# Kernel optimization log

Measured on AMD Instinct MI355X. Metric: run time of the kernel, lower is better.

## Reference

```python
import jax, jax.numpy as jnp
import numpy as np

BETA_MIN = 0.01
BETA_MAX = 0.995
EPS = 1e-6


def setup_inputs() -> dict:
    key = jax.random.key(0)
    k1, k2, k3, k4 = jax.random.split(key, 4)
    B, T, D = 16, 4096, 128
    return {
        "q": jax.random.normal(k1, (B, T, D), dtype=jnp.float32),
        "k": jax.random.normal(k2, (B, T, D), dtype=jnp.float32),
        "v": jax.random.normal(k3, (B, T, D), dtype=jnp.float32),
        "beta": jax.random.uniform(k4, (B, T, 1), dtype=jnp.float32),
        "mask": jnp.ones((B, T, 1), dtype=jnp.float32),
        "base_beta_1": jnp.asarray(2.0, dtype=jnp.float32),
        "base_beta_2": jnp.asarray(3.0, dtype=jnp.float32),
    }


def _delta_scan(q, k, v, beta, mask, base_beta_1, base_beta_2):
    B, T, D = q.shape
    phi_q = jax.nn.elu(q) + 1.0  # positive feature map
    phi_k = jax.nn.elu(k) + 1.0
    b1_base = jnp.clip(jax.nn.sigmoid(base_beta_1), BETA_MIN, BETA_MAX)
    b2_base = jnp.clip(jax.nn.sigmoid(base_beta_2), BETA_MIN, BETA_MAX)

    # time-major for scan: [T, B, ...]
    xs = (
        jnp.swapaxes(phi_q, 0, 1),
        jnp.swapaxes(phi_k, 0, 1),
        jnp.swapaxes(v, 0, 1),
        jnp.swapaxes(beta, 0, 1),
        jnp.swapaxes(mask, 0, 1),
    )

    H1 = jnp.zeros((B, D, D), dtype=q.dtype)
    H2 = jnp.zeros((B, D, D), dtype=q.dtype)
    Z1 = jnp.zeros((B, D), dtype=q.dtype)
    Z2 = jnp.zeros((B, D), dtype=q.dtype)

    def step(carry, x):
        H1, H2, Z1, Z2 = carry
        q_t, k_t, v_t, b_in_t, m_t = x  # q_t:[B,D], b_in_t/m_t:[B,1]
        b_in_t = jnp.clip(b_in_t, BETA_MIN, BETA_MAX)
        b1_t = jnp.clip(b1_base * b_in_t, BETA_MIN, BETA_MAX)  # [B,1]
        b2_t = jnp.clip(b2_base * b_in_t, BETA_MIN, BETA_MAX)
        kv = jnp.einsum('bd,be->bde', k_t, v_t) * m_t[:, :, None]  # masked outer product
        H1 = H1 * b1_t[:, :, None] + kv
        H2 = H2 * b2_t[:, :, None] + kv
        Z1 = Z1 * b1_t + k_t * m_t
        Z2 = Z2 * b2_t + k_t * m_t
        num = jnp.einsum('bd,bde->be', q_t, H1 + H2)
        den = jnp.maximum(jnp.sum(q_t * (Z1 + Z2), axis=-1, keepdims=True), EPS)
        o_t = num / den * m_t
        return (H1, H2, Z1, Z2), o_t

    _, outs = jax.lax.scan(step, (H1, H2, Z1, Z2), xs)
    return jnp.swapaxes(outs, 0, 1)  # [B, T, D]


def reference(q, k, v, beta, mask, base_beta_1, base_beta_2):
    return _delta_scan(q, k, v, beta, mask, base_beta_1, base_beta_2)
```

## Files before the change

### kernel.cpp

```cpp
#include <hip/hip_runtime.h>

#define B_ 16
#define T_ 4096
#define D_ 128
#define L_ 128
#define NC_ 32
#define CH_ (B_*NC_)
#define LDK 136
#define LDP 136

typedef __attribute__((ext_vector_type(8))) short bf16x8;
typedef __attribute__((ext_vector_type(4))) float f32x4;

__device__ __forceinline__ float clampf(float x, float lo, float hi) {
    return fminf(fmaxf(x, lo), hi);
}
__device__ __forceinline__ float phi_f(float x) {
    return x > 0.f ? x + 1.f : __expf(x);
}
__device__ __forceinline__ unsigned short bf16r(float f) {
    unsigned u = __builtin_bit_cast(unsigned, f);
    u += 0x7FFFu + ((u >> 16) & 1u);
    return (unsigned short)(u >> 16);
}
__device__ __forceinline__ float fbf(unsigned short h) {
    unsigned u = ((unsigned)h) << 16; return __builtin_bit_cast(float, u);
}
__device__ __forceinline__ unsigned pack2bf(float a, float b) {
    return (unsigned)bf16r(a) | ((unsigned)bf16r(b) << 16);
}
__device__ __forceinline__ uint4 pack8(const float* f) {
    uint4 r;
    r.x = pack2bf(f[0], f[1]); r.y = pack2bf(f[2], f[3]);
    r.z = pack2bf(f[4], f[5]); r.w = pack2bf(f[6], f[7]);
    return r;
}
__device__ __forceinline__ f32x4 zero4() { f32x4 z; z[0]=0.f; z[1]=0.f; z[2]=0.f; z[3]=0.f; return z; }


__global__ __launch_bounds__(256, 2) void kA(
        const float* __restrict__ beta,
        const float* __restrict__ bb1, const float* __restrict__ bb2,
        const float* __restrict__ kk, const float* __restrict__ vv,
        const float* __restrict__ mask,
        float* __restrict__ lg1, float* __restrict__ lg2,
        unsigned short* __restrict__ phiKT, unsigned short* __restrict__ VtT,
        unsigned short* __restrict__ Cws, float* __restrict__ zc) {
    int ch = blockIdx.x;
    int b = ch / NC_, c = ch % NC_;
    int tbase = b * T_ + c * L_;
    int tid = threadIdx.x, lane = tid & 63, w = tid >> 6;
    int l15 = lane & 15, lg4 = lane >> 4;
    size_t cb = (size_t)ch * (D_ * L_);

    __shared__ float s1[L_], s2[L_];
    __shared__ float wL[2][L_];
    __shared__ float sZp[2][256];
    __shared__ unsigned short sKrm[128 * LDK];
    __shared__ unsigned short sVrm[128 * LDK];

    int t = tid & 127;
    if (tid < 128) {
        float b1b = clampf(1.f / (1.f + __expf(-bb1[0])), 0.01f, 0.995f);
        float b2b = clampf(1.f / (1.f + __expf(-bb2[0])), 0.01f, 0.995f);
        float be = clampf(beta[tbase + t], 0.01f, 0.995f);
        s1[t] = __logf(clampf(b1b * be, 0.01f, 0.995f));
        s2[t] = __logf(clampf(b2b * be, 0.01f, 0.995f));
    }
    __syncthreads();
    for (int off = 1; off < L_; off <<= 1) {
        float a1 = 0.f, a2 = 0.f;
        if (tid < 128 && t >= off) { a1 = s1[t - off]; a2 = s2[t - off]; }
        __syncthreads();
        if (tid < 128) { s1[t] += a1; s2[t] += a2; }
        __syncthreads();
    }
    if (tid < 128) {
        lg1[tbase + t] = s1[t]; lg2[tbase + t] = s2[t];
        float tot1 = s1[L_ - 1], tot2 = s2[L_ - 1];
    }
    __syncthreads();
    if (tid < 128) {
        wL[0][t] = __expf(s1[L_ - 1] - s1[t]);
        wL[1][t] = __expf(s2[L_ - 1] - s2[t]);
    }

#pragma unroll
    for (int p = 0; p < 8; ++p) {
        int i = tid + p * 256;
        int s = i >> 4, dg = i & 15, d0 = dg * 8;
        const float* kp = &kk[(size_t)(tbase + s) * D_ + d0];
        float4 x0 = *(const float4*)kp;
        float4 x1 = *(const float4*)(kp + 4);
        float m = mask[tbase + s];
        float pq[8] = {phi_f(x0.x)*m, phi_f(x0.y)*m, phi_f(x0.z)*m, phi_f(x0.w)*m,
                       phi_f(x1.x)*m, phi_f(x1.y)*m, phi_f(x1.z)*m, phi_f(x1.w)*m};
        uint4 pk = pack8(pq);
        *(uint4*)&sKrm[s * LDK + d0] = pk;
        *(uint4*)&phiKT[cb + (size_t)((((s >> 4) * 4 + (d0 >> 5)) * 64 + ((d0 >> 3) & 3) * 16 + (s & 15)) * 8)] = pk;
    }
#pragma unroll
    for (int p = 0; p < 8; ++p) {
        int i = tid + p * 256;
        int s = i >> 4, eg = i & 15, e0 = eg * 8;
        const float* vp = &vv[(size_t)(tbase + s) * D_ + e0];
        float4 x0 = *(const float4*)vp;
        float4 x1 = *(const float4*)(vp + 4);
        float pv8[8] = {x0.x, x0.y, x0.z, x0.w, x1.x, x1.y, x1.z, x1.w};
        *(uint4*)&sVrm[s * LDK + e0] = pack8(pv8);
    }
    __syncthreads();

#pragma unroll
    for (int p = 0; p < 2; ++p) {
        int i = tid + p * 256;
        int mg = i >> 6, ln = i & 63;
        int vg4 = ln >> 4, v15 = ln & 15;
#pragma unroll
        for (int ks = 0; ks < 4; ++ks) {
            unsigned short u[8];
#pragma unroll
            for (int j = 0; j < 8; ++j)
                u[j] = sVrm[(ks * 32 + vg4 * 8 + j) * LDK + mg * 16 + v15];
            uint4 r;
            r.x = (unsigned)u[0] | ((unsigned)u[1] << 16);
            r.y = (unsigned)u[2] | ((unsigned)u[3] << 16);
            r.z = (unsigned)u[4] | ((unsigned)u[5] << 16);
            r.w = (unsigned)u[6] | ((unsigned)u[7] << 16);
            *(uint4*)&VtT[cb + (size_t)(((mg * 4 + ks) * 64 + ln) * 8)] = r;
        }
    }

    {
        int zd = tid & 127, zh = tid >> 7;
        float z0 = 0.f, z1 = 0.f;
#pragma unroll
        for (int ss = 0; ss < 64; ++ss) {
            int s = zh * 64 + ss;
            float kv = fbf(sKrm[s * LDK + zd]);
            z0 += wL[0][s] * kv;
            z1 += wL[1][s] * kv;
        }
        sZp[0][tid] = z0; sZp[1][tid] = z1;
    }

    f32x4 acc[2][2][8];
#pragma unroll
    for (int st = 0; st < 2; ++st)
#pragma unroll
        for (int mm = 0; mm < 2; ++mm)
#pragma unroll
            for (int n = 0; n < 8; ++n) acc[st][mm][n] = zero4();

#pragma unroll
    for (int ks = 0; ks < 4; ++ks) {
        int koff = ks * 32 + lg4 * 8;
        float4 w0a = *(const float4*)&wL[0][koff];
        float4 w0b = *(const float4*)&wL[0][koff + 4];
        float4 w1a = *(const float4*)&wL[1][koff];
        float4 w1b = *(const float4*)&wL[1][koff + 4];
        float wl0[8] = {w0a.x, w0a.y, w0a.z, w0a.w, w0b.x, w0b.y, w0b.z, w0b.w};
        float wl1[8] = {w1a.x, w1a.y, w1a.z, w1a.w, w1b.x, w1b.y, w1b.z, w1b.w};
        bf16x8 as[2][2];
#pragma unroll
        for (int mm = 0; mm < 2; ++mm) {
#pragma unroll
            for (int j = 0; j < 8; ++j) {
                float av = fbf(sVrm[(koff + j) * LDK + (w * 2 + mm) * 16 + l15]);
                as[0][mm][j] = (short)bf16r(av * wl0[j]);
                as[1][mm][j] = (short)bf16r(av * wl1[j]);
            }
        }
#pragma unroll
        for (int n = 0; n < 8; ++n) {
            bf16x8 bb;
#pragma unroll
            for (int j = 0; j < 8; ++j)
                bb[j] = (short)sKrm[(koff + j) * LDK + n * 16 + l15];
#pragma unroll
            for (int st = 0; st < 2; ++st)
#pragma unroll
                for (int mm = 0; mm < 2; ++mm)
                    acc[st][mm][n] = __builtin_amdgcn_mfma_f32_16x16x32_bf16(as[st][mm], bb, acc[st][mm][n], 0, 0, 0);
        }
    }
    __syncthreads();
    if (tid < 128) {
        zc[((size_t)(0 * B_ + b) * NC_ + c) * D_ + tid] = sZp[0][tid] + sZp[0][tid + 128];
        zc[((size_t)(1 * B_ + b) * NC_ + c) * D_ + tid] = sZp[1][tid] + sZp[1][tid + 128];
    }

#pragma unroll
    for (int st = 0; st < 2; ++st) {
        unsigned short* Cp = Cws + ((size_t)(st * B_ + b) * NC_ + c) * (D_ * D_);
#pragma unroll
        for (int mm = 0; mm < 2; ++mm)
#pragma unroll
            for (int n = 0; n < 8; ++n)
#pragma unroll
                for (int r = 0; r < 4; ++r) {
                    int e = (w * 2 + mm) * 16 + lg4 * 4 + r;
                    int d = n * 16 + l15;
                    Cp[(size_t)((((e >> 4) * 4 + (d >> 5)) * 64 + ((d >> 3) & 3) * 16 + (e & 15)) * 8 + (d & 7))] = bf16r(acc[st][mm][n][r]);
                }
    }
}

__global__ void k2f(unsigned short* __restrict__ Cws, float* __restrict__ zc,
                    const float* __restrict__ lg1, const float* __restrict__ lg2) {
    int g = blockIdx.x * blockDim.x + threadIdx.x;
    if (g < 131072) {
        int st = g >> 16;
        int rem = g & 65535;
        int b = rem >> 12;
        int de = (rem & 4095) * 4;
        const float* lg = st ? lg2 : lg1;
        size_t base = ((size_t)(st * B_ + b) * NC_) * (D_ * D_) + de;
        float run0 = 0.f, run1 = 0.f, run2 = 0.f, run3 = 0.f;
        for (int c = 0; c < NC_; c++) {
            float a = __expf(lg[b * T_ + c * L_ + L_ - 1]);
            uint2 val = *(uint2*)&Cws[base + (size_t)c * (D_ * D_)];
            float t0 = fbf((unsigned short)(val.x & 0xffff)), t1 = fbf((unsigned short)(val.x >> 16));
            float t2 = fbf((unsigned short)(val.y & 0xffff)), t3 = fbf((unsigned short)(val.y >> 16));
            uint2 wv; wv.x = pack2bf(run0, run1); wv.y = pack2bf(run2, run3);
            *(uint2*)&Cws[base + (size_t)c * (D_ * D_)] = wv;
            run0 = a * run0 + t0; run1 = a * run1 + t1;
            run2 = a * run2 + t2; run3 = a * run3 + t3;
        }
    } else {
        int gz = g - 131072;
        int st = gz >> 11;
        int rem = gz & 2047;
        int b = rem >> 7;
        int d = rem & 127;
        const float* lg = st ? lg2 : lg1;
        size_t base = ((size_t)(st * B_ + b) * NC_) * D_ + d;
        float run = 0.f;
        for (int c = 0; c < NC_; c++) {
            float a = __expf(lg[b * T_ + c * L_ + L_ - 1]);
            float tmp = zc[base + (size_t)c * D_];
            zc[base + (size_t)c * D_] = run;
            run = a * run + tmp;
        }
    }
}

__global__ __launch_bounds__(256, 2) void k3_v6(
        const float* __restrict__ qq, const float* __restrict__ mask,
        const float* __restrict__ lg1, const float* __restrict__ lg2,
        const unsigned short* __restrict__ phiKT, const unsigned short* __restrict__ VtT,
        const unsigned short* __restrict__ Cws, const float* __restrict__ zc,
        float* __restrict__ out) {
    __shared__ unsigned short bufP[4][32 * LDP];
    int ch = blockIdx.x;
    int b = ch / NC_, c = ch % NC_;
    int tbase = b * T_ + c * L_;
    int tid = threadIdx.x, lane = tid & 63, w = tid >> 6;
    int l15 = lane & 15, lg4 = lane >> 4;
    unsigned short* bufPw = &bufP[w][0];
    size_t cb = (size_t)ch * 16384;

    int trow0 = w * 16 + l15, trow1 = 64 + trow0;
    size_t gt0 = (size_t)(tbase + trow0), gt1 = (size_t)(tbase + trow1);

    float lg1t0 = lg1[gt0], lg2t0 = lg2[gt0], mt0 = mask[gt0];
    float lg1t1 = lg1[gt1], lg2t1 = lg2[gt1], mt1 = mask[gt1];
    float a1t0 = __expf(lg1t0), a2t0 = __expf(lg2t0);
    float a1t1 = __expf(lg1t1), a2t1 = __expf(lg2t1);

    bf16x8 qf0[4], qf1[4];
#pragma unroll
    for (int ks = 0; ks < 4; ++ks) {
        int koff = ks * 32 + lg4 * 8;
        const float* qp0 = &qq[gt0 * D_ + koff];
        const float* qp1 = &qq[gt1 * D_ + koff];
        float4 x0 = *(const float4*)qp0, x1 = *(const float4*)(qp0 + 4);
        float4 y0 = *(const float4*)qp1, y1 = *(const float4*)(qp1 + 4);
        float p0[8] = {phi_f(x0.x), phi_f(x0.y), phi_f(x0.z), phi_f(x0.w),
                       phi_f(x1.x), phi_f(x1.y), phi_f(x1.z), phi_f(x1.w)};
        float p1[8] = {phi_f(y0.x), phi_f(y0.y), phi_f(y0.z), phi_f(y0.w),
                       phi_f(y1.x), phi_f(y1.y), phi_f(y1.z), phi_f(y1.w)};
#pragma unroll
        for (int j = 0; j < 8; ++j) {
            qf0[ks][j] = (short)bf16r(p0[j]);
            qf1[ks][j] = (short)bf16r(p1[j]);
        }
    }

    const float* z1p = &zc[((size_t)(0 * B_ + b) * NC_ + c) * D_];
    const float* z2p = &zc[((size_t)(1 * B_ + b) * NC_ + c) * D_];
    float d1_0 = 0.f, d2_0 = 0.f, d1_1 = 0.f, d2_1 = 0.f;
#pragma unroll
    for (int ks = 0; ks < 4; ++ks) {
        int off = ks * 32 + lg4 * 8;
        float4 za = *(const float4*)(z1p + off), zb = *(const float4*)(z1p + off + 4);
        float4 zca = *(const float4*)(z2p + off), zcb = *(const float4*)(z2p + off + 4);
        float z1a[8] = {za.x, za.y, za.z, za.w, zb.x, zb.y, zb.z, zb.w};
        float z2a[8] = {zca.x, zca.y, zca.z, zca.w, zcb.x, zcb.y, zcb.z, zcb.w};
#pragma unroll
        for (int j = 0; j < 8; ++j) {
            float fq0 = fbf((unsigned short)qf0[ks][j]);
            float fq1 = fbf((unsigned short)qf1[ks][j]);
            d1_0 += fq0 * z1a[j]; d2_0 += fq0 * z2a[j];
            d1_1 += fq1 * z1a[j]; d2_1 += fq1 * z2a[j];
        }
    }
    d1_0 += __shfl_xor(d1_0, 16); d1_0 += __shfl_xor(d1_0, 32);
    d2_0 += __shfl_xor(d2_0, 16); d2_0 += __shfl_xor(d2_0, 32);
    d1_1 += __shfl_xor(d1_1, 16); d1_1 += __shfl_xor(d1_1, 32);
    d2_1 += __shfl_xor(d2_1, 16); d2_1 += __shfl_xor(d2_1, 32);

    float rs0 = 0.f, rs1 = 0.f;
#pragma unroll
    for (int mh = 0; mh < 2; ++mh) {
        bf16x8 kf[16];
#pragma unroll
        for (int mm = 0; mm < 4; ++mm)
#pragma unroll
            for (int ks = 0; ks < 4; ++ks)
                kf[mm * 4 + ks] = *(const bf16x8*)&phiKT[cb + (size_t)(((((mh * 4 + mm) * 4) + ks) * 64 + lane) * 8)];
        f32x4 acc0[4], acc1[4];
#pragma unroll
        for (int mm = 0; mm < 4; ++mm) { acc0[mm] = zero4(); acc1[mm] = zero4(); }
#pragma unroll
        for (int ks = 0; ks < 4; ++ks)
#pragma unroll
            for (int mm = 0; mm < 4; ++mm) {
                if (mh == 0)
                    acc0[mm] = __builtin_amdgcn_mfma_f32_16x16x32_bf16(kf[mm * 4 + ks], qf0[ks], acc0[mm], 0, 0, 0);
                acc1[mm] = __builtin_amdgcn_mfma_f32_16x16x32_bf16(kf[mm * 4 + ks], qf1[ks], acc1[mm], 0, 0, 0);
            }
#pragma unroll
        for (int mm = 0; mm < 4; ++mm) {
            int s0 = (mh * 4 + mm) * 16 + lg4 * 4;
            float4 l1s = *(const float4*)&lg1[tbase + s0];
            float4 l2s = *(const float4*)&lg2[tbase + s0];
            float l1a[4] = {l1s.x, l1s.y, l1s.z, l1s.w};
            float l2a[4] = {l2s.x, l2s.y, l2s.z, l2s.w};
            if (mh == 0) {
                float pv[4];
#pragma unroll
                for (int r = 0; r < 4; ++r) {
                    int s = s0 + r;
                    float p = 0.f;
                    if (s <= trow0)
                        p = acc0[mm][r] * (__expf(lg1t0 - l1a[r]) + __expf(lg2t0 - l2a[r]));
                    pv[r] = p; rs0 += p;
                }
                uint2 dd; dd.x = pack2bf(pv[0], pv[1]); dd.y = pack2bf(pv[2], pv[3]);
                *(uint2*)&bufPw[l15 * LDP + s0] = dd;
            }
            {
                float pv[4];
#pragma unroll
                for (int r = 0; r < 4; ++r) {
                    int s = s0 + r;
                    float p = 0.f;
                    if (s <= trow1)
                        p = acc1[mm][r] * (__expf(lg1t1 - l1a[r]) + __expf(lg2t1 - l2a[r]));
                    pv[r] = p; rs1 += p;
                }
                uint2 dd; dd.x = pack2bf(pv[0], pv[1]); dd.y = pack2bf(pv[2], pv[3]);
                *(uint2*)&bufPw[(16 + l15) * LDP + s0] = dd;
            }
        }
    }
    rs0 += __shfl_xor(rs0, 16); rs0 += __shfl_xor(rs0, 32);
    rs1 += __shfl_xor(rs1, 16); rs1 += __shfl_xor(rs1, 32);
    float osc0 = mt0 / fmaxf(a1t0 * d1_0 + a2t0 * d2_0 + rs0, 1e-6f);
    float osc1 = mt1 / fmaxf(a1t1 * d1_1 + a2t1 * d2_1 + rs1, 1e-6f);

    f32x4 acc_o0[8], acc_o1[8];
#pragma unroll
    for (int m = 0; m < 8; ++m) { acc_o0[m] = zero4(); acc_o1[m] = zero4(); }
#pragma unroll
    for (int st = 0; st < 2; ++st) {
        const unsigned short* Hp = Cws + ((size_t)(st * B_ + b) * NC_ + c) * (D_ * D_);
        float sc0 = st ? a2t0 : a1t0;
        float sc1 = st ? a2t1 : a1t1;
#pragma unroll
        for (int ks2 = 0; ks2 < 2; ++ks2) {
            bf16x8 hf[16];
#pragma unroll
            for (int kq = 0; kq < 2; ++kq)
#pragma unroll
                for (int m = 0; m < 8; ++m)
                    hf[kq * 8 + m] = *(const bf16x8*)&Hp[(size_t)(((m * 4 + ks2 * 2 + kq) * 64 + lane) * 8)];
#pragma unroll
            for (int kq = 0; kq < 2; ++kq) {
                int ks = ks2 * 2 + kq;
                bf16x8 qs0, qs1;
#pragma unroll
                for (int j = 0; j < 8; ++j) {
                    qs0[j] = (short)bf16r(fbf((unsigned short)qf0[ks][j]) * sc0);
                    qs1[j] = (short)bf16r(fbf((unsigned short)qf1[ks][j]) * sc1);
                }
#pragma unroll
                for (int m = 0; m < 8; ++m) {
                    acc_o0[m] = __builtin_amdgcn_mfma_f32_16x16x32_bf16(hf[kq * 8 + m], qs0, acc_o0[m], 0, 0, 0);
                    acc_o1[m] = __builtin_amdgcn_mfma_f32_16x16x32_bf16(hf[kq * 8 + m], qs1, acc_o1[m], 0, 0, 0);
                }
            }
        }
    }

#pragma unroll
    for (int ks = 0; ks < 4; ++ks) {
        bf16x8 vf[8];
#pragma unroll
        for (int m = 0; m < 8; ++m)
            vf[m] = *(const bf16x8*)&VtT[cb + (size_t)(((m * 4 + ks) * 64 + lane) * 8)];
        bf16x8 pf1 = *(const bf16x8*)&bufPw[(16 + l15) * LDP + ks * 32 + lg4 * 8];
        if (ks < 2) {
            bf16x8 pf0 = *(const bf16x8*)&bufPw[l15 * LDP + ks * 32 + lg4 * 8];
#pragma unroll
            for (int m = 0; m < 8; ++m)
                acc_o0[m] = __builtin_amdgcn_mfma_f32_16x16x32_bf16(vf[m], pf0, acc_o0[m], 0, 0, 0);
        }
#pragma unroll
        for (int m = 0; m < 8; ++m)
            acc_o1[m] = __builtin_amdgcn_mfma_f32_16x16x32_bf16(vf[m], pf1, acc_o1[m], 0, 0, 0);
    }

#pragma unroll
    for (int m = 0; m < 8; ++m) {
        float4 o0, o1;
        o0.x = acc_o0[m][0] * osc0; o0.y = acc_o0[m][1] * osc0;
        o0.z = acc_o0[m][2] * osc0; o0.w = acc_o0[m][3] * osc0;
        o1.x = acc_o1[m][0] * osc1; o1.y = acc_o1[m][1] * osc1;
        o1.z = acc_o1[m][2] * osc1; o1.w = acc_o1[m][3] * osc1;
        *(float4*)&out[gt0 * D_ + m * 16 + lg4 * 4] = o0;
        *(float4*)&out[gt1 * D_ + m * 16 + lg4 * 4] = o1;
    }
}

extern "C" void kernel_launch(void* const* d_in, const int* in_sizes, int n_in,
                              void* d_out, int out_size, void* d_ws, size_t ws_size,
                              hipStream_t stream) {
    const float* q    = (const float*)d_in[0];
    const float* k    = (const float*)d_in[1];
    const float* v    = (const float*)d_in[2];
    const float* beta = (const float*)d_in[3];
    const float* mask = (const float*)d_in[4];
    const float* bb1  = (const float*)d_in[5];
    const float* bb2  = (const float*)d_in[6];
    float* out = (float*)d_out;

    size_t n_lg = (size_t)B_ * T_;
    size_t n_z  = (size_t)2 * B_ * NC_ * D_;
    size_t n_C  = (size_t)2 * B_ * NC_ * D_ * D_;
    size_t n_kt = (size_t)B_ * T_ * D_;
    size_t need = (2 * n_lg + n_z) * sizeof(float) + (n_C + 2 * n_kt) * sizeof(unsigned short);
    if (ws_size < need) return;

    float* lg1 = (float*)d_ws;
    float* lg2 = lg1 + n_lg;
    float* zc  = lg2 + n_lg;
    unsigned short* Cws   = (unsigned short*)(zc + n_z);
    unsigned short* phiKT = Cws + n_C;
    unsigned short* VtT   = phiKT + n_kt;

    kA<<<CH_, 256, 0, stream>>>(beta, bb1, bb2, k, v, mask, lg1, lg2, phiKT, VtT, Cws, zc);
    k2f<<<528, 256, 0, stream>>>(Cws, zc, lg1, lg2);
    k3_v6<<<CH_, 256, 0, stream>>>(q, mask, lg1, lg2, phiKT, VtT, Cws, zc, out);
}
```

Before: 85.09 us.

## Transpose and XOR-swizzle chunk tiles in LDS, use wave-shuffle scan, stage C stores

Kernel A now stores phi(K) and V transposed in shared memory with an XOR swizzle. MFMA operands, the V transpose and the z reduction can then read 16-byte vectors instead of eight scalar strided reads. The log-decay prefix scan uses wave shuffles instead of a barrier-heavy shared-memory scan. The C outputs are first staged in shared memory, reusing the K/V buffers, and then written to global memory as coalesced 16-byte stores instead of scattered 2-byte stores. The costs are scalar 2-byte shared-memory writes during the transposed fill and an extra barrier.

```diff
diff --git a/kernel.cpp b/kernel.cpp
--- a/kernel.cpp
+++ b/kernel.cpp
@@ -8,6 +8,7 @@
 #define CH_ (B_*NC_)
 #define LDK 136
 #define LDP 136
+#define XS(row, scol) ((scol) ^ ((((row) >> 3) & 7) << 3))
 
 typedef __attribute__((ext_vector_type(8))) short bf16x8;
 typedef __attribute__((ext_vector_type(4))) float f32x4;
@@ -53,36 +54,38 @@
     int l15 = lane & 15, lg4 = lane >> 4;
     size_t cb = (size_t)ch * (D_ * L_);
 
-    __shared__ float s1[L_], s2[L_];
+    __shared__ float sL1[L_], sL2[L_];
     __shared__ float wL[2][L_];
-    __shared__ float sZp[2][256];
-    __shared__ unsigned short sKrm[128 * LDK];
-    __shared__ unsigned short sVrm[128 * LDK];
-
-    int t = tid & 127;
-    if (tid < 128) {
+    __shared__ float wtot[2][2];
+    __shared__ unsigned short sKt[128 * LDK];
+    __shared__ unsigned short sVt[128 * LDK];
+
+    if (w < 2) {
+        int t = w * 64 + lane;
         float b1b = clampf(1.f / (1.f + __expf(-bb1[0])), 0.01f, 0.995f);
         float b2b = clampf(1.f / (1.f + __expf(-bb2[0])), 0.01f, 0.995f);
         float be = clampf(beta[tbase + t], 0.01f, 0.995f);
-        s1[t] = __logf(clampf(b1b * be, 0.01f, 0.995f));
-        s2[t] = __logf(clampf(b2b * be, 0.01f, 0.995f));
-    }
-    __syncthreads();
-    for (int off = 1; off < L_; off <<= 1) {
-        float a1 = 0.f, a2 = 0.f;
-        if (tid < 128 && t >= off) { a1 = s1[t - off]; a2 = s2[t - off]; }
-        __syncthreads();
-        if (tid < 128) { s1[t] += a1; s2[t] += a2; }
-        __syncthreads();
-    }
-    if (tid < 128) {
-        lg1[tbase + t] = s1[t]; lg2[tbase + t] = s2[t];
-        float tot1 = s1[L_ - 1], tot2 = s2[L_ - 1];
+        float x1 = __logf(clampf(b1b * be, 0.01f, 0.995f));
+        float x2 = __logf(clampf(b2b * be, 0.01f, 0.995f));
+#pragma unroll
+        for (int off = 1; off < 64; off <<= 1) {
+            float y1 = __shfl_up(x1, off);
+            float y2 = __shfl_up(x2, off);
+            if (lane >= off) { x1 += y1; x2 += y2; }
+        }
+        if (lane == 63) { wtot[0][w] = x1; wtot[1][w] = x2; }
+        sL1[t] = x1; sL2[t] = x2;
     }
     __syncthreads();
     if (tid < 128) {
-        wL[0][t] = __expf(s1[L_ - 1] - s1[t]);
-        wL[1][t] = __expf(s2[L_ - 1] - s2[t]);
+        int t = tid;
+        float x1 = sL1[t], x2 = sL2[t];
+        if (t >= 64) { x1 += wtot[0][0]; x2 += wtot[1][0]; }
+        float tot1 = wtot[0][0] + wtot[0][1];
+        float tot2 = wtot[1][0] + wtot[1][1];
+        lg1[tbase + t] = x1; lg2[tbase + t] = x2;
+        wL[0][t] = __expf(tot1 - x1);
+        wL[1][t] = __expf(tot2 - x2);
     }
 
 #pragma unroll
@@ -90,24 +93,41 @@
         int i = tid + p * 256;
         int s = i >> 4, dg = i & 15, d0 = dg * 8;
         const float* kp = &kk[(size_t)(tbase + s) * D_ + d0];
-        float4 x0 = *(const float4*)kp;
-        float4 x1 = *(const float4*)(kp + 4);
+        float4 x0 = *(const float4*)kp, x1 = *(const float4*)(kp + 4);
         float m = mask[tbase + s];
         float pq[8] = {phi_f(x0.x)*m, phi_f(x0.y)*m, phi_f(x0.z)*m, phi_f(x0.w)*m,
                        phi_f(x1.x)*m, phi_f(x1.y)*m, phi_f(x1.z)*m, phi_f(x1.w)*m};
         uint4 pk = pack8(pq);
-        *(uint4*)&sKrm[s * LDK + d0] = pk;
         *(uint4*)&phiKT[cb + (size_t)((((s >> 4) * 4 + (d0 >> 5)) * 64 + ((d0 >> 3) & 3) * 16 + (s & 15)) * 8)] = pk;
+        unsigned short pu[8] = {
+            (unsigned short)(pk.x & 0xffff), (unsigned short)(pk.x >> 16),
+            (unsigned short)(pk.y & 0xffff), (unsigned short)(pk.y >> 16),
+            (unsigned short)(pk.z & 0xffff), (unsigned short)(pk.z >> 16),
+            (unsigned short)(pk.w & 0xffff), (unsigned short)(pk.w >> 16)};
+#pragma unroll
+        for (int j = 0; j < 8; ++j) {
+            int row = d0 + j;
+            sKt[row * LDK + XS(row, s)] = pu[j];
+        }
     }
 #pragma unroll
     for (int p = 0; p < 8; ++p) {
         int i = tid + p * 256;
         int s = i >> 4, eg = i & 15, e0 = eg * 8;
         const float* vp = &vv[(size_t)(tbase + s) * D_ + e0];
-        float4 x0 = *(const float4*)vp;
-        float4 x1 = *(const float4*)(vp + 4);
+        float4 x0 = *(const float4*)vp, x1 = *(const float4*)(vp + 4);
         float pv8[8] = {x0.x, x0.y, x0.z, x0.w, x1.x, x1.y, x1.z, x1.w};
-        *(uint4*)&sVrm[s * LDK + e0] = pack8(pv8);
+        uint4 pk = pack8(pv8);
+        unsigned short pu[8] = {
+            (unsigned short)(pk.x & 0xffff), (unsigned short)(pk.x >> 16),
+            (unsigned short)(pk.y & 0xffff), (unsigned short)(pk.y >> 16),
+            (unsigned short)(pk.z & 0xffff), (unsigned short)(pk.z >> 16),
+            (unsigned short)(pk.w & 0xffff), (unsigned short)(pk.w >> 16)};
+#pragma unroll
+        for (int j = 0; j < 8; ++j) {
+            int row = e0 + j;
+            sVt[row * LDK + XS(row, s)] = pu[j];
+        }
     }
     __syncthreads();
 
@@ -115,33 +135,28 @@
     for (int p = 0; p < 2; ++p) {
         int i = tid + p * 256;
         int mg = i >> 6, ln = i & 63;
-        int vg4 = ln >> 4, v15 = ln & 15;
+        int row = mg * 16 + (ln & 15);
 #pragma unroll
         for (int ks = 0; ks < 4; ++ks) {
-            unsigned short u[8];
-#pragma unroll
-            for (int j = 0; j < 8; ++j)
-                u[j] = sVrm[(ks * 32 + vg4 * 8 + j) * LDK + mg * 16 + v15];
-            uint4 r;
-            r.x = (unsigned)u[0] | ((unsigned)u[1] << 16);
-            r.y = (unsigned)u[2] | ((unsigned)u[3] << 16);
-            r.z = (unsigned)u[4] | ((unsigned)u[5] << 16);
-            r.w = (unsigned)u[6] | ((unsigned)u[7] << 16);
+            int col = ks * 32 + (ln >> 4) * 8;
+            uint4 r = *(const uint4*)&sVt[row * LDK + XS(row, col)];
             *(uint4*)&VtT[cb + (size_t)(((mg * 4 + ks) * 64 + ln) * 8)] = r;
         }
     }
 
     {
-        int zd = tid & 127, zh = tid >> 7;
-        float z0 = 0.f, z1 = 0.f;
-#pragma unroll
-        for (int ss = 0; ss < 64; ++ss) {
-            int s = zh * 64 + ss;
-            float kv = fbf(sKrm[s * LDK + zd]);
-            z0 += wL[0][s] * kv;
-            z1 += wL[1][s] * kv;
-        }
-        sZp[0][tid] = z0; sZp[1][tid] = z1;
+        int st = tid >> 7, d = tid & 127;
+        float acc = 0.f;
+#pragma unroll
+        for (int s8 = 0; s8 < 16; ++s8) {
+            uint4 kv = *(const uint4*)&sKt[d * LDK + XS(d, s8 * 8)];
+            const float* wp = &wL[st][s8 * 8];
+            acc += fbf((unsigned short)(kv.x & 0xffff)) * wp[0] + fbf((unsigned short)(kv.x >> 16)) * wp[1]
+                 + fbf((unsigned short)(kv.y & 0xffff)) * wp[2] + fbf((unsigned short)(kv.y >> 16)) * wp[3]
+                 + fbf((unsigned short)(kv.z & 0xffff)) * wp[4] + fbf((unsigned short)(kv.z >> 16)) * wp[5]
+                 + fbf((unsigned short)(kv.w & 0xffff)) * wp[6] + fbf((unsigned short)(kv.w >> 16)) * wp[7];
+        }
+        zc[((size_t)(st * B_ + b) * NC_ + c) * D_ + d] = acc;
     }
 
     f32x4 acc[2][2][8];
@@ -155,44 +170,44 @@
 #pragma unroll
     for (int ks = 0; ks < 4; ++ks) {
         int koff = ks * 32 + lg4 * 8;
-        float4 w0a = *(const float4*)&wL[0][koff];
-        float4 w0b = *(const float4*)&wL[0][koff + 4];
-        float4 w1a = *(const float4*)&wL[1][koff];
-        float4 w1b = *(const float4*)&wL[1][koff + 4];
-        float wl0[8] = {w0a.x, w0a.y, w0a.z, w0a.w, w0b.x, w0b.y, w0b.z, w0b.w};
-        float wl1[8] = {w1a.x, w1a.y, w1a.z, w1a.w, w1b.x, w1b.y, w1b.z, w1b.w};
-        bf16x8 as[2][2];
+        float wl0[8], wl1[8];
+        {
+            float4 a0 = *(const float4*)&wL[0][koff];
+            float4 a1 = *(const float4*)&wL[0][koff + 4];
+            float4 b0 = *(const float4*)&wL[1][koff];
+            float4 b1 = *(const float4*)&wL[1][koff + 4];
+            wl0[0]=a0.x; wl0[1]=a0.y; wl0[2]=a0.z; wl0[3]=a0.w;
+            wl0[4]=a1.x; wl0[5]=a1.y; wl0[6]=a1.z; wl0[7]=a1.w;
+            wl1[0]=b0.x; wl1[1]=b0.y; wl1[2]=b0.z; wl1[3]=b0.w;
+            wl1[4]=b1.x; wl1[5]=b1.y; wl1[6]=b1.z; wl1[7]=b1.w;
+        }
+        bf16x8 as0[2], as1[2];
 #pragma unroll
         for (int mm = 0; mm < 2; ++mm) {
+            int row = (w * 2 + mm) * 16 + l15;
+            bf16x8 vt = *(const bf16x8*)&sVt[row * LDK + XS(row, koff)];
 #pragma unroll
             for (int j = 0; j < 8; ++j) {
-                float av = fbf(sVrm[(koff + j) * LDK + (w * 2 + mm) * 16 + l15]);
-                as[0][mm][j] = (short)bf16r(av * wl0[j]);
-                as[1][mm][j] = (short)bf16r(av * wl1[j]);
+                float av = fbf((unsigned short)vt[j]);
+                as0[mm][j] = (short)bf16r(av * wl0[j]);
+                as1[mm][j] = (short)bf16r(av * wl1[j]);
             }
         }
 #pragma unroll
         for (int n = 0; n < 8; ++n) {
-            bf16x8 bb;
-#pragma unroll
-            for (int j = 0; j < 8; ++j)
-                bb[j] = (short)sKrm[(koff + j) * LDK + n * 16 + l15];
-#pragma unroll
-            for (int st = 0; st < 2; ++st)
-#pragma unroll
-                for (int mm = 0; mm < 2; ++mm)
-                    acc[st][mm][n] = __builtin_amdgcn_mfma_f32_16x16x32_bf16(as[st][mm], bb, acc[st][mm][n], 0, 0, 0);
+            int row = n * 16 + l15;
+            bf16x8 bb = *(const bf16x8*)&sKt[row * LDK + XS(row, koff)];
+            acc[0][0][n] = __builtin_amdgcn_mfma_f32_16x16x32_bf16(as0[0], bb, acc[0][0][n], 0, 0, 0);
+            acc[0][1][n] = __builtin_amdgcn_mfma_f32_16x16x32_bf16(as0[1], bb, acc[0][1][n], 0, 0, 0);
+            acc[1][0][n] = __builtin_amdgcn_mfma_f32_16x16x32_bf16(as1[0], bb, acc[1][0][n], 0, 0, 0);
+            acc[1][1][n] = __builtin_amdgcn_mfma_f32_16x16x32_bf16(as1[1], bb, acc[1][1][n], 0, 0, 0);
         }
     }
     __syncthreads();
-    if (tid < 128) {
-        zc[((size_t)(0 * B_ + b) * NC_ + c) * D_ + tid] = sZp[0][tid] + sZp[0][tid + 128];
-        zc[((size_t)(1 * B_ + b) * NC_ + c) * D_ + tid] = sZp[1][tid] + sZp[1][tid + 128];
-    }
 
 #pragma unroll
     for (int st = 0; st < 2; ++st) {
-        unsigned short* Cp = Cws + ((size_t)(st * B_ + b) * NC_ + c) * (D_ * D_);
+        unsigned short* basep = st ? sVt : sKt;
 #pragma unroll
         for (int mm = 0; mm < 2; ++mm)
 #pragma unroll
@@ -201,8 +216,19 @@
                 for (int r = 0; r < 4; ++r) {
                     int e = (w * 2 + mm) * 16 + lg4 * 4 + r;
                     int d = n * 16 + l15;
-                    Cp[(size_t)((((e >> 4) * 4 + (d >> 5)) * 64 + ((d >> 3) & 3) * 16 + (e & 15)) * 8 + (d & 7))] = bf16r(acc[st][mm][n][r]);
+                    basep[(((e >> 4) * 4 + (d >> 5)) * 64 + ((d >> 3) & 3) * 16 + (e & 15)) * 8 + (d & 7)] = bf16r(acc[st][mm][n][r]);
                 }
+    }
+    __syncthreads();
+#pragma unroll
+    for (int st = 0; st < 2; ++st) {
+        const unsigned short* basep = st ? sVt : sKt;
+        unsigned short* Cp = Cws + ((size_t)(st * B_ + b) * NC_ + c) * (D_ * D_);
+#pragma unroll
+        for (int p = 0; p < 8; ++p) {
+            int i = tid + p * 256;
+            *(uint4*)&Cp[(size_t)i * 8] = *(const uint4*)&basep[i * 8];
+        }
     }
 }
 
```

Result: faster. 78.38 us (-7.9%).

## Split chunk-state kernel into scan, staging and per-decay MFMA kernels

Applied to the files above, without the earlier changes.

Replaces the monolithic per-chunk kernel with three kernels. The first computes the log-decay prefix sums with wave shuffles instead of a shared-memory scan and writes the decay weights to global memory. The second packs phi(K), a transposed phi(K) and a transposed V into MFMA-ready bf16 layouts across four times as many blocks. The third runs the chunk-state MFMA with one decay per block (twice the grid) and stages the output through LDS for coalesced stores. This aims at more parallelism and lower register and LDS pressure, at the cost of extra launches and extra global traffic for the staged transposed copies.

```diff
diff --git a/kernel.cpp b/kernel.cpp
--- a/kernel.cpp
+++ b/kernel.cpp
@@ -6,7 +6,6 @@
 #define L_ 128
 #define NC_ 32
 #define CH_ (B_*NC_)
-#define LDK 136
 #define LDP 136
 
 typedef __attribute__((ext_vector_type(8))) short bf16x8;
@@ -37,172 +36,175 @@
 }
 __device__ __forceinline__ f32x4 zero4() { f32x4 z; z[0]=0.f; z[1]=0.f; z[2]=0.f; z[3]=0.f; return z; }
 
-
-__global__ __launch_bounds__(256, 2) void kA(
-        const float* __restrict__ beta,
-        const float* __restrict__ bb1, const float* __restrict__ bb2,
-        const float* __restrict__ kk, const float* __restrict__ vv,
-        const float* __restrict__ mask,
-        float* __restrict__ lg1, float* __restrict__ lg2,
-        unsigned short* __restrict__ phiKT, unsigned short* __restrict__ VtT,
-        unsigned short* __restrict__ Cws, float* __restrict__ zc) {
+__device__ __forceinline__ size_t aidx(int row, int k0) {
+    return (size_t)((((row >> 4) * 4 + (k0 >> 5)) * 64 + ((k0 >> 3) & 3) * 16 + (row & 15)) * 8);
+}
+
+__global__ void k0w(const float* __restrict__ beta,
+                    const float* __restrict__ bb1, const float* __restrict__ bb2,
+                    float* __restrict__ lg1, float* __restrict__ lg2,
+                    float* __restrict__ wexp) {
     int ch = blockIdx.x;
     int b = ch / NC_, c = ch % NC_;
     int tbase = b * T_ + c * L_;
-    int tid = threadIdx.x, lane = tid & 63, w = tid >> 6;
-    int l15 = lane & 15, lg4 = lane >> 4;
-    size_t cb = (size_t)ch * (D_ * L_);
-
-    __shared__ float s1[L_], s2[L_];
-    __shared__ float wL[2][L_];
-    __shared__ float sZp[2][256];
-    __shared__ unsigned short sKrm[128 * LDK];
-    __shared__ unsigned short sVrm[128 * LDK];
-
-    int t = tid & 127;
-    if (tid < 128) {
-        float b1b = clampf(1.f / (1.f + __expf(-bb1[0])), 0.01f, 0.995f);
-        float b2b = clampf(1.f / (1.f + __expf(-bb2[0])), 0.01f, 0.995f);
-        float be = clampf(beta[tbase + t], 0.01f, 0.995f);
-        s1[t] = __logf(clampf(b1b * be, 0.01f, 0.995f));
-        s2[t] = __logf(clampf(b2b * be, 0.01f, 0.995f));
-    }
+    int tid = threadIdx.x;
+    int lane = tid & 63, w = tid >> 6;
+    __shared__ float tot1s[2], tot2s[2];
+
+    float b1b = clampf(1.f / (1.f + __expf(-bb1[0])), 0.01f, 0.995f);
+    float b2b = clampf(1.f / (1.f + __expf(-bb2[0])), 0.01f, 0.995f);
+    float be = clampf(beta[tbase + tid], 0.01f, 0.995f);
+    float x1 = __logf(clampf(b1b * be, 0.01f, 0.995f));
+    float x2 = __logf(clampf(b2b * be, 0.01f, 0.995f));
+#pragma unroll
+    for (int off = 1; off < 64; off <<= 1) {
+        float y1 = __shfl_up(x1, off);
+        float y2 = __shfl_up(x2, off);
+        if (lane >= off) { x1 += y1; x2 += y2; }
+    }
+    if (lane == 63) { tot1s[w] = x1; tot2s[w] = x2; }
     __syncthreads();
-    for (int off = 1; off < L_; off <<= 1) {
-        float a1 = 0.f, a2 = 0.f;
-        if (tid < 128 && t >= off) { a1 = s1[t - off]; a2 = s2[t - off]; }
-        __syncthreads();
-        if (tid < 128) { s1[t] += a1; s2[t] += a2; }
-        __syncthreads();
-    }
-    if (tid < 128) {
-        lg1[tbase + t] = s1[t]; lg2[tbase + t] = s2[t];
-        float tot1 = s1[L_ - 1], tot2 = s2[L_ - 1];
-    }
-    __syncthreads();
-    if (tid < 128) {
-        wL[0][t] = __expf(s1[L_ - 1] - s1[t]);
-        wL[1][t] = __expf(s2[L_ - 1] - s2[t]);
-    }
-
-#pragma unroll
-    for (int p = 0; p < 8; ++p) {
-        int i = tid + p * 256;
-        int s = i >> 4, dg = i & 15, d0 = dg * 8;
+    if (w == 1) { x1 += tot1s[0]; x2 += tot2s[0]; }
+    float tot1 = tot1s[0] + tot1s[1];
+    float tot2 = tot2s[0] + tot2s[1];
+    lg1[tbase + tid] = x1;
+    lg2[tbase + tid] = x2;
+    wexp[(size_t)ch * 128 + tid]                  = __expf(tot1 - x1);
+    wexp[(size_t)CH_ * 128 + (size_t)ch * 128 + tid] = __expf(tot2 - x2);
+}
+
+__global__ __launch_bounds__(256) void kS(
+        const float* __restrict__ kk, const float* __restrict__ vv,
+        const float* __restrict__ mask,
+        unsigned short* __restrict__ phiKT, unsigned short* __restrict__ phiKtT,
+        unsigned short* __restrict__ VtT) {
+    int g = blockIdx.x;
+    int ch = g >> 2, q = g & 3;
+    int b = ch / NC_, c = ch % NC_;
+    int tbase = b * T_ + c * L_;
+    int tid = threadIdx.x;
+    size_t cb = (size_t)ch * 16384;
+
+#pragma unroll
+    for (int p = 0; p < 2; ++p) {
+        int i = p * 256 + tid;
+        int s = q * 32 + (i >> 4), d0 = (i & 15) * 8;
         const float* kp = &kk[(size_t)(tbase + s) * D_ + d0];
-        float4 x0 = *(const float4*)kp;
-        float4 x1 = *(const float4*)(kp + 4);
+        float4 x0 = *(const float4*)kp, x1 = *(const float4*)(kp + 4);
         float m = mask[tbase + s];
         float pq[8] = {phi_f(x0.x)*m, phi_f(x0.y)*m, phi_f(x0.z)*m, phi_f(x0.w)*m,
                        phi_f(x1.x)*m, phi_f(x1.y)*m, phi_f(x1.z)*m, phi_f(x1.w)*m};
-        uint4 pk = pack8(pq);
-        *(uint4*)&sKrm[s * LDK + d0] = pk;
-        *(uint4*)&phiKT[cb + (size_t)((((s >> 4) * 4 + (d0 >> 5)) * 64 + ((d0 >> 3) & 3) * 16 + (s & 15)) * 8)] = pk;
-    }
+        *(uint4*)&phiKT[cb + aidx(s, d0)] = pack8(pq);
+    }
+
+#pragma unroll
+    for (int p = 0; p < 2; ++p) {
+        int i = p * 256 + tid;
+        int d = q * 32 + (i & 31), s0 = (i >> 5) * 8;
+        const float* kp = &kk[(size_t)(tbase + s0) * D_ + d];
+        const float* mp = &mask[tbase + s0];
+        float f[8];
+#pragma unroll
+        for (int j = 0; j < 8; ++j)
+            f[j] = phi_f(kp[(size_t)j * D_]) * mp[j];
+        *(uint4*)&phiKtT[cb + aidx(d, s0)] = pack8(f);
+    }
+
+#pragma unroll
+    for (int p = 0; p < 2; ++p) {
+        int i = p * 256 + tid;
+        int e = q * 32 + (i & 31), s0 = (i >> 5) * 8;
+        const float* vp = &vv[(size_t)(tbase + s0) * D_ + e];
+        float f[8];
+#pragma unroll
+        for (int j = 0; j < 8; ++j)
+            f[j] = vp[(size_t)j * D_];
+        *(uint4*)&VtT[cb + aidx(e, s0)] = pack8(f);
+    }
+}
+
+__global__ __launch_bounds__(256, 2) void kC(
+        const unsigned short* __restrict__ phiKtT, const unsigned short* __restrict__ VtT,
+        const float* __restrict__ wexp,
+        unsigned short* __restrict__ Cws, float* __restrict__ zc) {
+    int ch = blockIdx.x, st = blockIdx.y;
+    int b = ch / NC_, c = ch % NC_;
+    int tid = threadIdx.x, lane = tid & 63, w = tid >> 6;
+    int l15 = lane & 15, lg4 = lane >> 4;
+    size_t cb = (size_t)ch * 16384;
+    __shared__ unsigned short sC[16384];
+
+    const float* wp = &wexp[(size_t)st * CH_ * 128 + (size_t)ch * 128];
+    float wv[4][8];
+#pragma unroll
+    for (int ks = 0; ks < 4; ++ks) {
+        float4 a0 = *(const float4*)&wp[ks * 32 + lg4 * 8];
+        float4 a1 = *(const float4*)&wp[ks * 32 + lg4 * 8 + 4];
+        wv[ks][0] = a0.x; wv[ks][1] = a0.y; wv[ks][2] = a0.z; wv[ks][3] = a0.w;
+        wv[ks][4] = a1.x; wv[ks][5] = a1.y; wv[ks][6] = a1.z; wv[ks][7] = a1.w;
+    }
+
+    f32x4 acc[2][8];
+#pragma unroll
+    for (int mm = 0; mm < 2; ++mm)
+#pragma unroll
+        for (int n = 0; n < 8; ++n) acc[mm][n] = zero4();
+    float zp[8] = {0.f, 0.f, 0.f, 0.f, 0.f, 0.f, 0.f, 0.f};
+
+#pragma unroll
+    for (int ks = 0; ks < 4; ++ks) {
+        bf16x8 as[2];
+#pragma unroll
+        for (int mm = 0; mm < 2; ++mm) {
+            bf16x8 vt = *(const bf16x8*)&VtT[cb + (size_t)((((w * 2 + mm) * 4 + ks) * 64 + lane) * 8)];
+#pragma unroll
+            for (int j = 0; j < 8; ++j)
+                as[mm][j] = (short)bf16r(fbf((unsigned short)vt[j]) * wv[ks][j]);
+        }
+        bf16x8 bb[8];
+#pragma unroll
+        for (int n = 0; n < 8; ++n)
+            bb[n] = *(const bf16x8*)&phiKtT[cb + (size_t)(((n * 4 + ks) * 64 + lane) * 8)];
+        if (w == 0) {
+#pragma unroll
+            for (int n = 0; n < 8; ++n)
+#pragma unroll
+                for (int j = 0; j < 8; ++j)
+                    zp[n] += wv[ks][j] * fbf((unsigned short)bb[n][j]);
+        }
+#pragma unroll
+        for (int n = 0; n < 8; ++n) {
+            acc[0][n] = __builtin_amdgcn_mfma_f32_16x16x32_bf16(as[0], bb[n], acc[0][n], 0, 0, 0);
+            acc[1][n] = __builtin_amdgcn_mfma_f32_16x16x32_bf16(as[1], bb[n], acc[1][n], 0, 0, 0);
+        }
+    }
+
+    if (w == 0) {
+#pragma unroll
+        for (int n = 0; n < 8; ++n) {
+            float z = zp[n];
+            z += __shfl_xor(z, 16); z += __shfl_xor(z, 32);
+            if (lg4 == 0)
+                zc[((size_t)(st * B_ + b) * NC_ + c) * D_ + n * 16 + l15] = z;
+        }
+    }
+
+#pragma unroll
+    for (int mm = 0; mm < 2; ++mm)
+#pragma unroll
+        for (int n = 0; n < 8; ++n)
+#pragma unroll
+            for (int r = 0; r < 4; ++r) {
+                int e = (w * 2 + mm) * 16 + lg4 * 4 + r;
+                int d = n * 16 + l15;
+                sC[aidx(e, d & ~7) + (d & 7)] = bf16r(acc[mm][n][r]);
+            }
+    __syncthreads();
+    unsigned short* Cp = Cws + ((size_t)(st * B_ + b) * NC_ + c) * (D_ * D_);
 #pragma unroll
     for (int p = 0; p < 8; ++p) {
         int i = tid + p * 256;
-        int s = i >> 4, eg = i & 15, e0 = eg * 8;
-        const float* vp = &vv[(size_t)(tbase + s) * D_ + e0];
-        float4 x0 = *(const float4*)vp;
-        float4 x1 = *(const float4*)(vp + 4);
-        float pv8[8] = {x0.x, x0.y, x0.z, x0.w, x1.x, x1.y, x1.z, x1.w};
-        *(uint4*)&sVrm[s * LDK + e0] = pack8(pv8);
-    }
-    __syncthreads();
-
-#pragma unroll
-    for (int p = 0; p < 2; ++p) {
-        int i = tid + p * 256;
-        int mg = i >> 6, ln = i & 63;
-        int vg4 = ln >> 4, v15 = ln & 15;
-#pragma unroll
-        for (int ks = 0; ks < 4; ++ks) {
-            unsigned short u[8];
-#pragma unroll
-            for (int j = 0; j < 8; ++j)
-                u[j] = sVrm[(ks * 32 + vg4 * 8 + j) * LDK + mg * 16 + v15];
-            uint4 r;
-            r.x = (unsigned)u[0] | ((unsigned)u[1] << 16);
-            r.y = (unsigned)u[2] | ((unsigned)u[3] << 16);
-            r.z = (unsigned)u[4] | ((unsigned)u[5] << 16);
-            r.w = (unsigned)u[6] | ((unsigned)u[7] << 16);
-            *(uint4*)&VtT[cb + (size_t)(((mg * 4 + ks) * 64 + ln) * 8)] = r;
-        }
-    }
-
-    {
-        int zd = tid & 127, zh = tid >> 7;
-        float z0 = 0.f, z1 = 0.f;
-#pragma unroll
-        for (int ss = 0; ss < 64; ++ss) {
-            int s = zh * 64 + ss;
-            float kv = fbf(sKrm[s * LDK + zd]);
-            z0 += wL[0][s] * kv;
-            z1 += wL[1][s] * kv;
-        }
-        sZp[0][tid] = z0; sZp[1][tid] = z1;
-    }
-
-    f32x4 acc[2][2][8];
-#pragma unroll
-    for (int st = 0; st < 2; ++st)
-#pragma unroll
-        for (int mm = 0; mm < 2; ++mm)
-#pragma unroll
-            for (int n = 0; n < 8; ++n) acc[st][mm][n] = zero4();
-
-#pragma unroll
-    for (int ks = 0; ks < 4; ++ks) {
-        int koff = ks * 32 + lg4 * 8;
-        float4 w0a = *(const float4*)&wL[0][koff];
-        float4 w0b = *(const float4*)&wL[0][koff + 4];
-        float4 w1a = *(const float4*)&wL[1][koff];
-        float4 w1b = *(const float4*)&wL[1][koff + 4];
-        float wl0[8] = {w0a.x, w0a.y, w0a.z, w0a.w, w0b.x, w0b.y, w0b.z, w0b.w};
-        float wl1[8] = {w1a.x, w1a.y, w1a.z, w1a.w, w1b.x, w1b.y, w1b.z, w1b.w};
-        bf16x8 as[2][2];
-#pragma unroll
-        for (int mm = 0; mm < 2; ++mm) {
-#pragma unroll
-            for (int j = 0; j < 8; ++j) {
-                float av = fbf(sVrm[(koff + j) * LDK + (w * 2 + mm) * 16 + l15]);
-                as[0][mm][j] = (short)bf16r(av * wl0[j]);
-                as[1][mm][j] = (short)bf16r(av * wl1[j]);
-            }
-        }
-#pragma unroll
-        for (int n = 0; n < 8; ++n) {
-            bf16x8 bb;
-#pragma unroll
-            for (int j = 0; j < 8; ++j)
-                bb[j] = (short)sKrm[(koff + j) * LDK + n * 16 + l15];
-#pragma unroll
-            for (int st = 0; st < 2; ++st)
-#pragma unroll
-                for (int mm = 0; mm < 2; ++mm)
-                    acc[st][mm][n] = __builtin_amdgcn_mfma_f32_16x16x32_bf16(as[st][mm], bb, acc[st][mm][n], 0, 0, 0);
-        }
-    }
-    __syncthreads();
-    if (tid < 128) {
-        zc[((size_t)(0 * B_ + b) * NC_ + c) * D_ + tid] = sZp[0][tid] + sZp[0][tid + 128];
-        zc[((size_t)(1 * B_ + b) * NC_ + c) * D_ + tid] = sZp[1][tid] + sZp[1][tid + 128];
-    }
-
-#pragma unroll
-    for (int st = 0; st < 2; ++st) {
-        unsigned short* Cp = Cws + ((size_t)(st * B_ + b) * NC_ + c) * (D_ * D_);
-#pragma unroll
-        for (int mm = 0; mm < 2; ++mm)
-#pragma unroll
-            for (int n = 0; n < 8; ++n)
-#pragma unroll
-                for (int r = 0; r < 4; ++r) {
-                    int e = (w * 2 + mm) * 16 + lg4 * 4 + r;
-                    int d = n * 16 + l15;
-                    Cp[(size_t)((((e >> 4) * 4 + (d >> 5)) * 64 + ((d >> 3) & 3) * 16 + (e & 15)) * 8 + (d & 7))] = bf16r(acc[st][mm][n][r]);
-                }
+        *(uint4*)&Cp[(size_t)i * 8] = *(const uint4*)&sC[i * 8];
     }
 }
 
@@ -448,19 +450,24 @@
 
     size_t n_lg = (size_t)B_ * T_;
     size_t n_z  = (size_t)2 * B_ * NC_ * D_;
+    size_t n_w  = (size_t)2 * CH_ * 128;
     size_t n_C  = (size_t)2 * B_ * NC_ * D_ * D_;
     size_t n_kt = (size_t)B_ * T_ * D_;
-    size_t need = (2 * n_lg + n_z) * sizeof(float) + (n_C + 2 * n_kt) * sizeof(unsigned short);
+    size_t need = (2 * n_lg + n_z + n_w) * sizeof(float) + (n_C + 3 * n_kt) * sizeof(unsigned short);
     if (ws_size < need) return;
 
-    float* lg1 = (float*)d_ws;
-    float* lg2 = lg1 + n_lg;
-    float* zc  = lg2 + n_lg;
-    unsigned short* Cws   = (unsigned short*)(zc + n_z);
-    unsigned short* phiKT = Cws + n_C;
-    unsigned short* VtT   = phiKT + n_kt;
-
-    kA<<<CH_, 256, 0, stream>>>(beta, bb1, bb2, k, v, mask, lg1, lg2, phiKT, VtT, Cws, zc);
+    float* lg1  = (float*)d_ws;
+    float* lg2  = lg1 + n_lg;
+    float* zc   = lg2 + n_lg;
+    float* wexp = zc + n_z;
+    unsigned short* Cws    = (unsigned short*)(wexp + n_w);
+    unsigned short* phiKT  = Cws + n_C;
+    unsigned short* phiKtT = phiKT + n_kt;
+    unsigned short* VtT    = phiKtT + n_kt;
+
+    k0w<<<CH_, 128, 0, stream>>>(beta, bb1, bb2, lg1, lg2, wexp);
+    kS<<<4 * CH_, 256, 0, stream>>>(k, v, mask, phiKT, phiKtT, VtT);
+    kC<<<dim3(CH_, 2), 256, 0, stream>>>(phiKtT, VtT, wexp, Cws, zc);
     k2f<<<528, 256, 0, stream>>>(Cws, zc, lg1, lg2);
     k3_v6<<<CH_, 256, 0, stream>>>(q, mask, lg1, lg2, phiKT, VtT, Cws, zc, out);
 }
```

New measurement: 99.35 us. +16.8%, slower.
